# Optimization experiments

Hardware: AMD Instinct MI355X
Metric: run time of the kernel (lower is better)

The kernel has to match this reference:

```python
import jax, jax.numpy as jnp
import numpy as np

DIM = 1024
H_MID = max(8, DIM // 2)   # 512
H_LOW = max(8, DIM // 4)   # 256


def setup_inputs() -> dict:
    key = jax.random.key(0)
    ks = jax.random.split(key, 10)
    s = lambda fan_in: 1.0 / np.sqrt(fan_in)
    x = jax.random.normal(ks[0], (4, 8192, DIM), dtype=jnp.float32)
    return {
        "x": x,
        "gamma": jnp.ones((DIM,), jnp.float32),
        "beta": jnp.zeros((DIM,), jnp.float32),
        "W1": jax.random.uniform(ks[1], (DIM, H_MID), jnp.float32, -s(DIM), s(DIM)),
        "b1": jax.random.uniform(ks[2], (H_MID,), jnp.float32, -s(DIM), s(DIM)),
        "W2": jax.random.uniform(ks[3], (H_MID, H_MID), jnp.float32, -s(H_MID), s(H_MID)),
        "b2": jax.random.uniform(ks[4], (H_MID,), jnp.float32, -s(H_MID), s(H_MID)),
        "W3": jax.random.uniform(ks[5], (H_MID, H_LOW), jnp.float32, -s(H_MID), s(H_MID)),
        "b3": jax.random.uniform(ks[6], (H_LOW,), jnp.float32, -s(H_MID), s(H_MID)),
        "W4": jax.random.uniform(ks[7], (H_LOW, DIM), jnp.float32, -s(H_LOW), s(H_LOW)),
        "b4": jax.random.uniform(ks[8], (DIM,), jnp.float32, -s(H_LOW), s(H_LOW)),
    }


def _layernorm(x, gamma, beta, eps=1e-5):
    mu = jnp.mean(x, axis=-1, keepdims=True)
    var = jnp.mean(jnp.square(x - mu), axis=-1, keepdims=True)
    return (x - mu) * jax.lax.rsqrt(var + eps) * gamma + beta


def reference(x, gamma, beta, W1, b1, W2, b2, W3, b3, W4, b4):
    gelu = lambda h: jax.nn.gelu(h, approximate=False)  # torch default: exact erf GELU
    h = _layernorm(x, gamma, beta)                      # (B,S,D)
    h = gelu(jnp.einsum("bsd,dm->bsm", h, W1) + b1)    # (B,S,D/2)
    h = gelu(jnp.einsum("bsm,mn->bsn", h, W2) + b2)    # (B,S,D/2)
    h = gelu(jnp.einsum("bsn,nl->bsl", h, W3) + b3)    # (B,S,D/4)
    h = jnp.einsum("bsl,ld->bsd", h, W4) + b4          # (B,S,D)
    return x + h
```

## Files before the change

kernel.cpp:

```cpp
#include <hip/hip_runtime.h>


typedef short short8 __attribute__((ext_vector_type(8)));
typedef float floatx4 __attribute__((ext_vector_type(4)));
typedef unsigned short ushort4v __attribute__((ext_vector_type(4)));
typedef unsigned int uint2v __attribute__((ext_vector_type(2)));

__device__ __forceinline__ unsigned short f2bf(float f) {
    union { float f; unsigned int u; } a; a.f = f;
    unsigned int u = a.u;
    return (unsigned short)((u + 0x7FFFu + ((u >> 16) & 1u)) >> 16);
}

__device__ __forceinline__ float bf2f(unsigned short h) {
    union { unsigned int u; float f; } a; a.u = ((unsigned int)h) << 16;
    return a.f;
}

__device__ __forceinline__ unsigned int pkbf(float a, float b) {
    return (unsigned int)f2bf(a) | ((unsigned int)f2bf(b) << 16);
}

__device__ __forceinline__ float gelu_fast(float v) {
    float u = 0.7978845608f * v * (1.0f + 0.044715f * v * v);
    float e = __builtin_amdgcn_exp2f(u * 2.885390082f);
    float t = 1.0f - 2.0f * __builtin_amdgcn_rcpf(1.0f + e);
    return 0.5f * v * (1.0f + t);
}

__device__ __forceinline__ void gl_lds16(const unsigned short* g, unsigned short* l) {
    __builtin_amdgcn_global_load_lds(
        (const __attribute__((address_space(1))) void*)g,
        (__attribute__((address_space(3))) void*)l, 16, 0, 0);
}

#define BARX() asm volatile("s_barrier" ::: "memory")
#define VMW8() asm volatile("s_waitcnt vmcnt(8)" ::: "memory")
#define VMW4() asm volatile("s_waitcnt vmcnt(4)" ::: "memory")
#define VMW0() asm volatile("s_waitcnt vmcnt(0)" ::: "memory")

__global__ __launch_bounds__(256) void conv_all_kernel(
    const float* __restrict__ W1, const float* __restrict__ W2,
    const float* __restrict__ W3, const float* __restrict__ W4,
    const float* __restrict__ gamma, const float* __restrict__ b1,
    unsigned short* __restrict__ Wt1, unsigned short* __restrict__ Wt2,
    unsigned short* __restrict__ Wt3, unsigned short* __restrict__ Wt4,
    float* __restrict__ u1, float* __restrict__ c1) {
    int b = blockIdx.x;
    if (b >= 4608) {
        int n = (b - 4608) * 256 + threadIdx.x;
        u1[n] = 0.f;
        c1[n] = b1[n];
        return;
    }
    const float* W; unsigned short* Wt; int K, N; const float* sc = nullptr;
    if (b < 2048)      { W = W1; Wt = Wt1; K = 1024; N = 512;  sc = gamma; }
    else if (b < 3072) { W = W2; Wt = Wt2; K = 512;  N = 512;  b -= 2048; }
    else if (b < 3584) { W = W3; Wt = Wt3; K = 512;  N = 256;  b -= 3072; }
    else               { W = W4; Wt = Wt4; K = 256;  N = 1024; b -= 3584; }
    int t = b * 256 + threadIdx.x;
    int sh = 31 - __clz(N);
    int k = t >> sh, n = t & (N - 1);
    float v = W[t];
    if (sc) v *= sc[k];
    Wt[(size_t)n * K + k] = f2bf(v);
}

__global__ __launch_bounds__(256) void u1c1_kernel(
    const float* __restrict__ W1, const float* __restrict__ gamma,
    const float* __restrict__ beta, float* __restrict__ u1,
    float* __restrict__ c1) {
    const int N = 512;
    __shared__ float gs[16], bs[16];
    int n = threadIdx.x;
    int k0 = blockIdx.x * 16;
    if (n < 16) { gs[n] = gamma[k0 + n]; bs[n] = beta[k0 + n]; }
    __syncthreads();
    float ua = 0.f, ca = 0.f, ub = 0.f, cb = 0.f;
#pragma unroll
    for (int i = 0; i < 16; i++) {
        float w0 = W1[(size_t)(k0 + i) * N + n];
        float w1 = W1[(size_t)(k0 + i) * N + n + 256];
        ua += gs[i] * w0; ca += bs[i] * w0;
        ub += gs[i] * w1; cb += bs[i] * w1;
    }
    atomicAdd(&u1[n], ua);       atomicAdd(&c1[n], ca);
    atomicAdd(&u1[n + 256], ub); atomicAdd(&c1[n + 256], cb);
}

__global__ __launch_bounds__(256) void ln_stats_kernel(
    const float* __restrict__ x, float* __restrict__ mu, float* __restrict__ rs,
    unsigned short* __restrict__ xb) {
    const int D = 1024;
    int row = blockIdx.x * 4 + (threadIdx.x >> 6);
    int lane = threadIdx.x & 63;
    const float4* xr = (const float4*)(x + (size_t)row * D);
    float s = 0.f, ss = 0.f;
#pragma unroll
    for (int i = 0; i < 4; i++) {
        float4 v = xr[lane + 64 * i];
        s  += v.x + v.y + v.z + v.w;
        ss += v.x * v.x + v.y * v.y + v.z * v.z + v.w * v.w;
        if (xb) {
            ushort4v o;
            o.x = f2bf(v.x); o.y = f2bf(v.y); o.z = f2bf(v.z); o.w = f2bf(v.w);
            *(ushort4v*)(xb + (size_t)row * D + 4 * (lane + 64 * i)) = o;
        }
    }
#pragma unroll
    for (int off = 32; off; off >>= 1) {
        s  += __shfl_xor(s, off);
        ss += __shfl_xor(ss, off);
    }
    if (lane == 0) {
        float m = s * (1.0f / 1024.0f);
        mu[row] = m;
        rs[row] = rsqrtf(ss * (1.0f / 1024.0f) - m * m + 1e-5f);
    }
}

__device__ __forceinline__ void ldA8(const unsigned short* base, short8 (&a)[8]) {
#pragma unroll
    for (int mt = 0; mt < 8; mt++) a[mt] = *(const short8*)(base + mt * 512);
}
__device__ __forceinline__ void ldB2(const unsigned short* base, short8 (&bb)[2]) {
    bb[0] = *(const short8*)(base);
    bb[1] = *(const short8*)(base + 512);
}
template <int CH>
__device__ __forceinline__ void mm16(const short8 (&a)[8], const short8 (&bb)[2],
                                     floatx4 (&acc)[8][4]) {
    __builtin_amdgcn_s_setprio(1);
#pragma unroll
    for (int mt = 0; mt < 8; mt++)
#pragma unroll
        for (int nt = 0; nt < 2; nt++)
            acc[mt][CH * 2 + nt] = __builtin_amdgcn_mfma_f32_16x16x32_bf16(
                bb[nt], a[mt], acc[mt][CH * 2 + nt], 0, 0, 0);
    __builtin_amdgcn_s_setprio(0);
}

template <int KLEN, int MODE>
__device__ __forceinline__ void do_tile(
    const unsigned short* aF0, const unsigned short* bF0,
    const unsigned short* aF1, const unsigned short* bF1,
    unsigned short* sA3, unsigned short* sB3,
    unsigned short* sA4, unsigned short* sB4,
    const unsigned short* gAs, const unsigned short* gBs,
    short8 (&a)[8], short8 (&bb)[2], floatx4 (&acc)[8][4]) {
    ldA8(aF0, a);
    ldB2(bF0, bb);
    if (MODE <= 1) {
        gl_lds16(gAs + 96, sA3);
        gl_lds16(gAs + 96 + (size_t)128 * KLEN, sA3 + 4096);
    }
    mm16<0>(a, bb, acc);
    BARX();
    ldB2(bF0 + 1024, bb);
    if (MODE <= 1) {
        gl_lds16(gBs + 96, sB3);
        gl_lds16(gBs + 96 + (size_t)128 * KLEN, sB3 + 4096);
    }
    mm16<1>(a, bb, acc);
    if (MODE <= 1) { VMW8(); } else { VMW0(); }
    BARX();
    ldA8(aF1, a);
    ldB2(bF1, bb);
    if (MODE == 0) {
        gl_lds16(gAs + 128, sA4);
        gl_lds16(gAs + 128 + (size_t)128 * KLEN, sA4 + 4096);
    }
    mm16<0>(a, bb, acc);
    BARX();
    ldB2(bF1 + 1024, bb);
    if (MODE == 0) {
        gl_lds16(gBs + 128, sB4);
        gl_lds16(gBs + 128 + (size_t)128 * KLEN, sB4 + 4096);
    }
    mm16<1>(a, bb, acc);
    if (MODE == 0) { VMW8(); }
    else if (MODE == 1) { VMW4(); }
    BARX();
}

template <int EPMODE, int NBN, int NT, int NOUT, int KLEN>
__global__ __launch_bounds__(512, 2) void gemm256_kernel(
    const unsigned short* __restrict__ A, const unsigned short* __restrict__ Bt,
    unsigned short* __restrict__ Out,
    const float* __restrict__ bias,
    const float* __restrict__ u1,
    const float* __restrict__ mu,
    const float* __restrict__ rs)
{
    __shared__ unsigned short lds[4][2][8192];

    const int tid  = threadIdx.x;
    const int wave = tid >> 6;
    const int lane = tid & 63;
    const int q    = lane >> 4;
    const int l16  = lane & 15;
    const int wm   = wave >> 2;
    const int wn   = wave & 3;

    const int id   = blockIdx.x;
    const int xcd  = id & 7;
    const int slot = id >> 3;
    const int m0   = (xcd + 8 * (slot / NBN)) * 256;
    const int n0   = (slot % NBN) * 256;

    const unsigned short* gAs = A  + (size_t)(m0 + (tid >> 2)) * KLEN + (tid & 3) * 8;
    const unsigned short* gBs = Bt + (size_t)(n0 + (tid >> 2)) * KLEN + (tid & 3) * 8;

    const int wo = wave << 9;
    unsigned short* sA[4]; unsigned short* sB[4];
    const unsigned short* fA[4]; const unsigned short* fB[4];
    const int aoff = (wm * 128 + l16) * 32 + q * 8;
    const int boff = (wn * 64 + l16) * 32 + q * 8;
#pragma unroll
    for (int s = 0; s < 4; s++) {
        sA[s] = &lds[s][0][0] + wo;
        sB[s] = &lds[s][1][0] + wo;
        fA[s] = &lds[s][0][0] + aoff;
        fB[s] = &lds[s][1][0] + boff;
    }

    floatx4 acc[8][4] = {};
    short8 a[8], bb[2];

    gl_lds16(gAs,      sA[0]); gl_lds16(gAs      + (size_t)128 * KLEN, sA[0] + 4096);
    gl_lds16(gBs,      sB[0]); gl_lds16(gBs      + (size_t)128 * KLEN, sB[0] + 4096);
    gl_lds16(gAs + 32, sA[1]); gl_lds16(gAs + 32 + (size_t)128 * KLEN, sA[1] + 4096);
    gl_lds16(gBs + 32, sB[1]); gl_lds16(gBs + 32 + (size_t)128 * KLEN, sB[1] + 4096);
    gl_lds16(gAs + 64, sA[2]); gl_lds16(gAs + 64 + (size_t)128 * KLEN, sA[2] + 4096);
    gl_lds16(gBs + 64, sB[2]); gl_lds16(gBs + 64 + (size_t)128 * KLEN, sB[2] + 4096);
    VMW8();
    BARX();

    for (int t = 0; t + 2 < NT; t += 2) {
        do_tile<KLEN, 0>(fA[0], fB[0], fA[1], fB[1], sA[3], sB[3], sA[0], sB[0],
                         gAs, gBs, a, bb, acc);
        gAs += 64; gBs += 64;
        do_tile<KLEN, 0>(fA[2], fB[2], fA[3], fB[3], sA[1], sB[1], sA[2], sB[2],
                         gAs, gBs, a, bb, acc);
        gAs += 64; gBs += 64;
    }
    do_tile<KLEN, 1>(fA[0], fB[0], fA[1], fB[1], sA[3], sB[3], sA[0], sB[0],
                     gAs, gBs, a, bb, acc);
    gAs += 64; gBs += 64;
    do_tile<KLEN, 2>(fA[2], fB[2], fA[3], fB[3], sA[1], sB[1], sA[2], sB[2],
                     gAs, gBs, a, bb, acc);

    float rs8[8], mu8[8];
    if constexpr (EPMODE == 0) {
#pragma unroll
        for (int ma = 0; ma < 8; ma++) {
            const int row = m0 + wm * 128 + ma * 16 + l16;
            rs8[ma] = rs[row];
            mu8[ma] = mu[row];
        }
    }
#pragma unroll
    for (int na = 0; na < 4; na++) {
        const int nb = n0 + wn * 64 + na * 16 + q * 4;
        const float4 bv = *(const float4*)(bias + nb);
        float4 uv = {0.f, 0.f, 0.f, 0.f};
        if constexpr (EPMODE == 0) uv = *(const float4*)(u1 + nb);
#pragma unroll
        for (int ma = 0; ma < 8; ma++) {
            const int row = m0 + wm * 128 + ma * 16 + l16;
            const size_t off = (size_t)row * NOUT + nb;
            float v0 = acc[ma][na][0], v1 = acc[ma][na][1];
            float v2 = acc[ma][na][2], v3 = acc[ma][na][3];
            if constexpr (EPMODE == 0) {
                v0 = gelu_fast(rs8[ma] * (v0 - mu8[ma] * uv.x) + bv.x);
                v1 = gelu_fast(rs8[ma] * (v1 - mu8[ma] * uv.y) + bv.y);
                v2 = gelu_fast(rs8[ma] * (v2 - mu8[ma] * uv.z) + bv.z);
                v3 = gelu_fast(rs8[ma] * (v3 - mu8[ma] * uv.w) + bv.w);
            } else {
                v0 = gelu_fast(v0 + bv.x);
                v1 = gelu_fast(v1 + bv.y);
                v2 = gelu_fast(v2 + bv.z);
                v3 = gelu_fast(v3 + bv.w);
            }
            uint2v o; o.x = pkbf(v0, v1); o.y = pkbf(v2, v3);
            *(uint2v*)(Out + off) = o;
        }
    }
}

template <int EPMODE, bool AF32, int NBN, int NT_, int KT>
__global__ __launch_bounds__(256) void gemm_kernel(
    const void* __restrict__ Aptr, const unsigned short* __restrict__ Bt,
    void* __restrict__ Out,
    const float* __restrict__ bias,
    const float* __restrict__ u1,
    const float* __restrict__ mu,
    const float* __restrict__ rs,
    const void* __restrict__ resid)
{
    constexpr int BM = 128, BN = 128, BK = 64;
    constexpr int N = NT_, K = KT;
    __shared__ unsigned short As[BM][BK];
    __shared__ unsigned short Bs[BN][BK];

    const int tid  = threadIdx.x;
    const int wave = tid >> 6;
    const int lane = tid & 63;
    const int q    = lane >> 4;
    const int l16  = lane & 15;
    const int wm   = wave & 1;
    const int wn   = wave >> 1;

    const int id   = blockIdx.x;
    const int xcd  = id & 7;
    const int slot = id >> 3;
    const int m0   = (xcd + 8 * (slot / NBN)) * BM;
    const int n0   = (slot % NBN) * BN;

    const int sr  = tid >> 3;
    const int sc  = tid & 7;
    const int sg  = sc ^ (sr & 7);
    unsigned short* lA = &As[0][0] + (wave << 9);
    unsigned short* lB = &Bs[0][0] + (wave << 9);
    const unsigned short* gb0 = Bt + (size_t)(n0 + sr) * K + sg * 8;
    const unsigned short* ga0 = nullptr;
    if (!AF32) ga0 = (const unsigned short*)Aptr + (size_t)(m0 + sr) * K + sg * 8;

    floatx4 acc[4][4] = {};

#pragma unroll
    for (int k0 = 0; k0 < K; k0 += BK) {
        if (AF32) {
            const float* A = (const float*)Aptr;
            int c = tid & 15, r0 = tid >> 4;
#pragma unroll
            for (int i = 0; i < 8; i++) {
                int r = r0 + 16 * i;
                float4 v = *(const float4*)(A + (size_t)(m0 + r) * K + k0 + c * 4);
                ushort4v o;
                o.x = f2bf(v.x); o.y = f2bf(v.y);
                o.z = f2bf(v.z); o.w = f2bf(v.w);
                int idx = r * 64 + (((c >> 1) ^ (r & 7)) << 3) + ((c & 1) << 2);
                *(ushort4v*)(&As[0][0] + idx) = o;
            }
        } else {
#pragma unroll
            for (int c = 0; c < 4; c++)
                gl_lds16(ga0 + k0 + (size_t)(32 * c) * K, lA + c * 2048);
        }
#pragma unroll
        for (int c = 0; c < 4; c++)
            gl_lds16(gb0 + k0 + (size_t)(32 * c) * K, lB + c * 2048);
        __syncthreads();

#pragma unroll
        for (int kk = 0; kk < 2; kk++) {
            const int gsw = ((kk * 4 + q) ^ (l16 & 7)) * 8;
            short8 a[4], b[4];
#pragma unroll
            for (int mt = 0; mt < 4; mt++)
                a[mt] = *(const short8*)(&As[0][0] + (wm * 64 + mt * 16 + l16) * 64 + gsw);
#pragma unroll
            for (int nt = 0; nt < 4; nt++)
                b[nt] = *(const short8*)(&Bs[0][0] + (wn * 64 + nt * 16 + l16) * 64 + gsw);
#pragma unroll
            for (int nt = 0; nt < 4; nt++)
#pragma unroll
                for (int mt = 0; mt < 4; mt++)
                    acc[nt][mt] = __builtin_amdgcn_mfma_f32_16x16x32_bf16(
                        b[nt], a[mt], acc[nt][mt], 0, 0, 0);
        }
        __syncthreads();
    }

    float rs4[4], mu4[4];
    if constexpr (EPMODE == 0) {
#pragma unroll
        for (int mt = 0; mt < 4; mt++) {
            const int row = m0 + wm * 64 + mt * 16 + l16;
            rs4[mt] = rs[row];
            mu4[mt] = mu[row];
        }
    }
#pragma unroll
    for (int nt = 0; nt < 4; nt++) {
        const int nbase = n0 + wn * 64 + nt * 16 + q * 4;
        const float4 bv = *(const float4*)(bias + nbase);
        float4 uv = {0.f, 0.f, 0.f, 0.f};
        if constexpr (EPMODE == 0) uv = *(const float4*)(u1 + nbase);
#pragma unroll
        for (int mt = 0; mt < 4; mt++) {
            const int row = m0 + wm * 64 + mt * 16 + l16;
            const size_t off = (size_t)row * N + nbase;
            float v0 = acc[nt][mt][0], v1 = acc[nt][mt][1];
            float v2 = acc[nt][mt][2], v3 = acc[nt][mt][3];
            if constexpr (EPMODE == 0) {
                v0 = gelu_fast(rs4[mt] * (v0 - mu4[mt] * uv.x) + bv.x);
                v1 = gelu_fast(rs4[mt] * (v1 - mu4[mt] * uv.y) + bv.y);
                v2 = gelu_fast(rs4[mt] * (v2 - mu4[mt] * uv.z) + bv.z);
                v3 = gelu_fast(rs4[mt] * (v3 - mu4[mt] * uv.w) + bv.w);
                uint2v o; o.x = pkbf(v0, v1); o.y = pkbf(v2, v3);
                *(uint2v*)((unsigned short*)Out + off) = o;
            } else if constexpr (EPMODE == 1) {
                v0 = gelu_fast(v0 + bv.x);
                v1 = gelu_fast(v1 + bv.y);
                v2 = gelu_fast(v2 + bv.z);
                v3 = gelu_fast(v3 + bv.w);
                uint2v o; o.x = pkbf(v0, v1); o.y = pkbf(v2, v3);
                *(uint2v*)((unsigned short*)Out + off) = o;
            } else if constexpr (EPMODE == 2) {
                const float4 rv = *(const float4*)((const float*)resid + off);
                float4 o;
                o.x = v0 + bv.x + rv.x;
                o.y = v1 + bv.y + rv.y;
                o.z = v2 + bv.z + rv.z;
                o.w = v3 + bv.w + rv.w;
                *(float4*)((float*)Out + off) = o;
            } else {
                const ushort4v rv =
                    *(const ushort4v*)((const unsigned short*)resid + off);
                float4 o;
                o.x = v0 + bv.x + bf2f(rv.x);
                o.y = v1 + bv.y + bf2f(rv.y);
                o.z = v2 + bv.z + bf2f(rv.z);
                o.w = v3 + bv.w + bf2f(rv.w);
                *(float4*)((float*)Out + off) = o;
            }
        }
    }
}

extern "C" void kernel_launch(void* const* d_in, const int* in_sizes, int n_in,
                              void* d_out, int out_size, void* d_ws, size_t ws_size,
                              hipStream_t stream) {
    const float* x     = (const float*)d_in[0];
    const float* gamma = (const float*)d_in[1];
    const float* beta  = (const float*)d_in[2];
    const float* W1    = (const float*)d_in[3];
    const float* b1    = (const float*)d_in[4];
    const float* W2    = (const float*)d_in[5];
    const float* b2    = (const float*)d_in[6];
    const float* W3    = (const float*)d_in[7];
    const float* b3    = (const float*)d_in[8];
    const float* W4    = (const float*)d_in[9];
    const float* b4    = (const float*)d_in[10];
    float* out = (float*)d_out;

    const int D = 1024, H1 = 512, H2 = 512;
    const int M = in_sizes[0] / D;

    char* ws = (char*)d_ws;
    unsigned short* Wt1 = (unsigned short*)(ws + 0);
    unsigned short* Wt2 = (unsigned short*)(ws + 1048576);
    unsigned short* Wt3 = (unsigned short*)(ws + 1572864);
    unsigned short* Wt4 = (unsigned short*)(ws + 1835008);
    float* u1           = (float*)(ws + 2359296);
    float* c1           = (float*)(ws + 2361344);
    float* muv          = (float*)(ws + 2363392);
    float* rsv          = (float*)(ws + 2494464);
    unsigned short* h1  = (unsigned short*)(ws + 2625536);
    unsigned short* h2  = (unsigned short*)(ws + 36179968);
    unsigned short* h3  = h1;
    size_t base_end     = 36179968 + (size_t)M * H2 * 2;
    unsigned short* xb  = (unsigned short*)(ws + base_end);
    bool use_xb = (ws_size >= base_end + (size_t)M * D * 2);

    const int NBM = M / 128;

    conv_all_kernel<<<4610, 256, 0, stream>>>(W1, W2, W3, W4, gamma, b1,
                                              Wt1, Wt2, Wt3, Wt4, u1, c1);
    u1c1_kernel<<<D / 16, 256, 0, stream>>>(W1, gamma, beta, u1, c1);

    ln_stats_kernel<<<M / 4, 256, 0, stream>>>(x, muv, rsv, use_xb ? xb : nullptr);

    if (use_xb) {
        gemm256_kernel<0, 2, 16, 512, 1024><<<(M / 256) * 2, 512, 0, stream>>>(
            xb, Wt1, h1, c1, u1, muv, rsv);
    } else {
        gemm_kernel<0, true, 4, 512, 1024><<<4 * NBM, 256, 0, stream>>>(
            x, Wt1, h1, c1, u1, muv, rsv, nullptr);
    }
    gemm256_kernel<1, 2, 8, 512, 512><<<(M / 256) * 2, 512, 0, stream>>>(
        h1, Wt2, h2, b2, nullptr, nullptr, nullptr);
    gemm_kernel<1, false, 2, 256, 512><<<2 * NBM, 256, 0, stream>>>(
        h2, Wt3, h3, b3, nullptr, nullptr, nullptr, nullptr);
    if (use_xb) {
        gemm_kernel<3, false, 8, 1024, 256><<<8 * NBM, 256, 0, stream>>>(
            h3, Wt4, out, b4, nullptr, nullptr, nullptr, xb);
    } else {
        gemm_kernel<2, false, 8, 1024, 256><<<8 * NBM, 256, 0, stream>>>(
            h3, Wt4, out, b4, nullptr, nullptr, nullptr, x);
    }
}
```

Baseline: 399.0 us.

## Fuse GEMM2 and GEMM3 through LDS and merge LN stats into prep kernel

Adds a gemm23 kernel in which each 128-row block computes the full GELU(h1·W2+b2) tile into 128KB of LDS, then immediately multiplies it by W3 to produce h3. This removes the global round trip of the h2 intermediate and one launch. Separately, the layernorm-stats/bf16-cast work is folded into the weight-conversion kernel as extra blocks, which saves another launch. The fused GEMM is single-buffered with BK=32 and two barriers per step, and runs only one block per CU over M/128 blocks. That may make it less efficient than the previously tuned gemm256 path.

Result: no change. 404.0 us (+1.2%).

```diff
diff --git a/kernel.cpp b/kernel.cpp
--- a/kernel.cpp
+++ b/kernel.cpp
@@ -39,31 +39,63 @@
 #define VMW4() asm volatile("s_waitcnt vmcnt(4)" ::: "memory")
 #define VMW0() asm volatile("s_waitcnt vmcnt(0)" ::: "memory")
 
-__global__ __launch_bounds__(256) void conv_all_kernel(
+__global__ __launch_bounds__(256) void prep_kernel(
     const float* __restrict__ W1, const float* __restrict__ W2,
     const float* __restrict__ W3, const float* __restrict__ W4,
     const float* __restrict__ gamma, const float* __restrict__ b1,
+    const float* __restrict__ x,
     unsigned short* __restrict__ Wt1, unsigned short* __restrict__ Wt2,
     unsigned short* __restrict__ Wt3, unsigned short* __restrict__ Wt4,
-    float* __restrict__ u1, float* __restrict__ c1) {
+    float* __restrict__ u1, float* __restrict__ c1,
+    float* __restrict__ mu, float* __restrict__ rs,
+    unsigned short* __restrict__ xb) {
     int b = blockIdx.x;
-    if (b >= 4608) {
+    if (b < 4608) {
+        const float* W; unsigned short* Wt; int K, N; const float* sc = nullptr;
+        if (b < 2048)      { W = W1; Wt = Wt1; K = 1024; N = 512;  sc = gamma; }
+        else if (b < 3072) { W = W2; Wt = Wt2; K = 512;  N = 512;  b -= 2048; }
+        else if (b < 3584) { W = W3; Wt = Wt3; K = 512;  N = 256;  b -= 3072; }
+        else               { W = W4; Wt = Wt4; K = 256;  N = 1024; b -= 3584; }
+        int t = b * 256 + threadIdx.x;
+        int sh = 31 - __clz(N);
+        int k = t >> sh, n = t & (N - 1);
+        float v = W[t];
+        if (sc) v *= sc[k];
+        Wt[(size_t)n * K + k] = f2bf(v);
+        return;
+    }
+    if (b < 4610) {
         int n = (b - 4608) * 256 + threadIdx.x;
         u1[n] = 0.f;
         c1[n] = b1[n];
         return;
     }
-    const float* W; unsigned short* Wt; int K, N; const float* sc = nullptr;
-    if (b < 2048)      { W = W1; Wt = Wt1; K = 1024; N = 512;  sc = gamma; }
-    else if (b < 3072) { W = W2; Wt = Wt2; K = 512;  N = 512;  b -= 2048; }
-    else if (b < 3584) { W = W3; Wt = Wt3; K = 512;  N = 256;  b -= 3072; }
-    else               { W = W4; Wt = Wt4; K = 256;  N = 1024; b -= 3584; }
-    int t = b * 256 + threadIdx.x;
-    int sh = 31 - __clz(N);
-    int k = t >> sh, n = t & (N - 1);
-    float v = W[t];
-    if (sc) v *= sc[k];
-    Wt[(size_t)n * K + k] = f2bf(v);
+    const int D = 1024;
+    int row = (b - 4610) * 4 + (threadIdx.x >> 6);
+    int lane = threadIdx.x & 63;
+    const float4* xr = (const float4*)(x + (size_t)row * D);
+    float s = 0.f, ss = 0.f;
+#pragma unroll
+    for (int i = 0; i < 4; i++) {
+        float4 v = xr[lane + 64 * i];
+        s  += v.x + v.y + v.z + v.w;
+        ss += v.x * v.x + v.y * v.y + v.z * v.z + v.w * v.w;
+        if (xb) {
+            ushort4v o;
+            o.x = f2bf(v.x); o.y = f2bf(v.y); o.z = f2bf(v.z); o.w = f2bf(v.w);
+            *(ushort4v*)(xb + (size_t)row * D + 4 * (lane + 64 * i)) = o;
+        }
+    }
+#pragma unroll
+    for (int off = 32; off; off >>= 1) {
+        s  += __shfl_xor(s, off);
+        ss += __shfl_xor(ss, off);
+    }
+    if (lane == 0) {
+        float m = s * (1.0f / 1024.0f);
+        mu[row] = m;
+        rs[row] = rsqrtf(ss * (1.0f / 1024.0f) - m * m + 1e-5f);
+    }
 }
 
 __global__ __launch_bounds__(256) void u1c1_kernel(
@@ -86,37 +118,6 @@
     }
     atomicAdd(&u1[n], ua);       atomicAdd(&c1[n], ca);
     atomicAdd(&u1[n + 256], ub); atomicAdd(&c1[n + 256], cb);
-}
-
-__global__ __launch_bounds__(256) void ln_stats_kernel(
-    const float* __restrict__ x, float* __restrict__ mu, float* __restrict__ rs,
-    unsigned short* __restrict__ xb) {
-    const int D = 1024;
-    int row = blockIdx.x * 4 + (threadIdx.x >> 6);
-    int lane = threadIdx.x & 63;
-    const float4* xr = (const float4*)(x + (size_t)row * D);
-    float s = 0.f, ss = 0.f;
-#pragma unroll
-    for (int i = 0; i < 4; i++) {
-        float4 v = xr[lane + 64 * i];
-        s  += v.x + v.y + v.z + v.w;
-        ss += v.x * v.x + v.y * v.y + v.z * v.z + v.w * v.w;
-        if (xb) {
-            ushort4v o;
-            o.x = f2bf(v.x); o.y = f2bf(v.y); o.z = f2bf(v.z); o.w = f2bf(v.w);
-            *(ushort4v*)(xb + (size_t)row * D + 4 * (lane + 64 * i)) = o;
-        }
-    }
-#pragma unroll
-    for (int off = 32; off; off >>= 1) {
-        s  += __shfl_xor(s, off);
-        ss += __shfl_xor(ss, off);
-    }
-    if (lane == 0) {
-        float m = s * (1.0f / 1024.0f);
-        mu[row] = m;
-        rs[row] = rsqrtf(ss * (1.0f / 1024.0f) - m * m + 1e-5f);
-    }
 }
 
 __device__ __forceinline__ void ldA8(const unsigned short* base, short8 (&a)[8]) {
@@ -284,6 +285,112 @@
             }
             uint2v o; o.x = pkbf(v0, v1); o.y = pkbf(v2, v3);
             *(uint2v*)(Out + off) = o;
+        }
+    }
+}
+
+__global__ __launch_bounds__(512, 2) void gemm23_kernel(
+    const unsigned short* __restrict__ h1, const unsigned short* __restrict__ Wt2,
+    const unsigned short* __restrict__ Wt3, unsigned short* __restrict__ h3,
+    const float* __restrict__ b2, const float* __restrict__ b3)
+{
+    __shared__ unsigned short h2s[65536];
+    __shared__ unsigned short stg[8192];
+    const int tid  = threadIdx.x;
+    const int wave = tid >> 6, lane = tid & 63;
+    const int q = lane >> 4, l16 = lane & 15;
+    const int wm = wave >> 2, wn = wave & 3;
+    const int m0 = blockIdx.x * 128;
+    const int sr2 = tid >> 2, pg2 = tid & 3;
+    const int sg2 = pg2 ^ (sr2 & 3);
+    unsigned short* stW0 = stg + wave * 512;
+    unsigned short* stW1 = stg + 4096 + wave * 512;
+    const int x2 = (q ^ (l16 & 3)) * 8;
+
+    floatx4 acc[4][4];
+    short8 a[4], bb[4];
+
+    for (int nt4 = 0; nt4 < 4; nt4++) {
+#pragma unroll
+        for (int mt = 0; mt < 4; mt++)
+#pragma unroll
+            for (int nt = 0; nt < 2; nt++)
+                acc[mt][nt] = (floatx4){0.f, 0.f, 0.f, 0.f};
+        for (int ks = 0; ks < 16; ks++) {
+            gl_lds16(h1  + (size_t)(m0 + sr2) * 512        + ks * 32 + sg2 * 8, stW0);
+            gl_lds16(Wt2 + (size_t)(nt4 * 128 + sr2) * 512 + ks * 32 + sg2 * 8, stW1);
+            __syncthreads();
+#pragma unroll
+            for (int mt = 0; mt < 4; mt++)
+                a[mt] = *(const short8*)(stg + (wm * 64 + mt * 16 + l16) * 32 + x2);
+#pragma unroll
+            for (int nt = 0; nt < 2; nt++)
+                bb[nt] = *(const short8*)(stg + 4096 + (wn * 32 + nt * 16 + l16) * 32 + x2);
+#pragma unroll
+            for (int mt = 0; mt < 4; mt++)
+#pragma unroll
+                for (int nt = 0; nt < 2; nt++)
+                    acc[mt][nt] = __builtin_amdgcn_mfma_f32_16x16x32_bf16(
+                        bb[nt], a[mt], acc[mt][nt], 0, 0, 0);
+            __syncthreads();
+        }
+#pragma unroll
+        for (int nt = 0; nt < 2; nt++) {
+            const int col = nt4 * 128 + wn * 32 + nt * 16 + q * 4;
+            const float4 bv = *(const float4*)(b2 + col);
+#pragma unroll
+            for (int mt = 0; mt < 4; mt++) {
+                const int row = wm * 64 + mt * 16 + l16;
+                float v0 = gelu_fast(acc[mt][nt][0] + bv.x);
+                float v1 = gelu_fast(acc[mt][nt][1] + bv.y);
+                float v2 = gelu_fast(acc[mt][nt][2] + bv.z);
+                float v3 = gelu_fast(acc[mt][nt][3] + bv.w);
+                const int phys = (col >> 3) ^ (l16 & 7);
+                uint2v o; o.x = pkbf(v0, v1); o.y = pkbf(v2, v3);
+                *(uint2v*)(h2s + row * 512 + phys * 8 + (q & 1) * 4) = o;
+            }
+        }
+    }
+
+#pragma unroll
+    for (int mt = 0; mt < 4; mt++)
+#pragma unroll
+        for (int nt = 0; nt < 4; nt++)
+            acc[mt][nt] = (floatx4){0.f, 0.f, 0.f, 0.f};
+    for (int ks = 0; ks < 16; ks++) {
+        gl_lds16(Wt3 + (size_t)(sr2) * 512       + ks * 32 + sg2 * 8, stW0);
+        gl_lds16(Wt3 + (size_t)(sr2 + 128) * 512 + ks * 32 + sg2 * 8, stW1);
+        __syncthreads();
+#pragma unroll
+        for (int mt = 0; mt < 4; mt++) {
+            const int row = wm * 64 + mt * 16 + l16;
+            const int phys = (ks * 4 + q) ^ (l16 & 7);
+            a[mt] = *(const short8*)(h2s + row * 512 + phys * 8);
+        }
+#pragma unroll
+        for (int nt = 0; nt < 4; nt++)
+            bb[nt] = *(const short8*)(stg + (wn * 64 + nt * 16 + l16) * 32 + x2);
+#pragma unroll
+        for (int mt = 0; mt < 4; mt++)
+#pragma unroll
+            for (int nt = 0; nt < 4; nt++)
+                acc[mt][nt] = __builtin_amdgcn_mfma_f32_16x16x32_bf16(
+                    bb[nt], a[mt], acc[mt][nt], 0, 0, 0);
+        __syncthreads();
+    }
+#pragma unroll
+    for (int nt = 0; nt < 4; nt++) {
+        const int col = wn * 64 + nt * 16 + q * 4;
+        const float4 bv = *(const float4*)(b3 + col);
+#pragma unroll
+        for (int mt = 0; mt < 4; mt++) {
+            const int row = m0 + wm * 64 + mt * 16 + l16;
+            float v0 = gelu_fast(acc[mt][nt][0] + bv.x);
+            float v1 = gelu_fast(acc[mt][nt][1] + bv.y);
+            float v2 = gelu_fast(acc[mt][nt][2] + bv.z);
+            float v3 = gelu_fast(acc[mt][nt][3] + bv.w);
+            uint2v o; o.x = pkbf(v0, v1); o.y = pkbf(v2, v3);
+            *(uint2v*)(h3 + (size_t)row * 256 + col) = o;
         }
     }
 }
@@ -459,20 +566,17 @@
     float* muv          = (float*)(ws + 2363392);
     float* rsv          = (float*)(ws + 2494464);
     unsigned short* h1  = (unsigned short*)(ws + 2625536);
-    unsigned short* h2  = (unsigned short*)(ws + 36179968);
-    unsigned short* h3  = h1;
+    unsigned short* h3  = (unsigned short*)(ws + 36179968);
     size_t base_end     = 36179968 + (size_t)M * H2 * 2;
     unsigned short* xb  = (unsigned short*)(ws + base_end);
     bool use_xb = (ws_size >= base_end + (size_t)M * D * 2);
 
     const int NBM = M / 128;
 
-    conv_all_kernel<<<4610, 256, 0, stream>>>(W1, W2, W3, W4, gamma, b1,
-                                              Wt1, Wt2, Wt3, Wt4, u1, c1);
+    prep_kernel<<<4610 + M / 4, 256, 0, stream>>>(
+        W1, W2, W3, W4, gamma, b1, x, Wt1, Wt2, Wt3, Wt4,
+        u1, c1, muv, rsv, use_xb ? xb : nullptr);
     u1c1_kernel<<<D / 16, 256, 0, stream>>>(W1, gamma, beta, u1, c1);
-
-    ln_stats_kernel<<<M / 4, 256, 0, stream>>>(x, muv, rsv, use_xb ? xb : nullptr);
-
     if (use_xb) {
         gemm256_kernel<0, 2, 16, 512, 1024><<<(M / 256) * 2, 512, 0, stream>>>(
             xb, Wt1, h1, c1, u1, muv, rsv);
@@ -480,10 +584,7 @@
         gemm_kernel<0, true, 4, 512, 1024><<<4 * NBM, 256, 0, stream>>>(
             x, Wt1, h1, c1, u1, muv, rsv, nullptr);
     }
-    gemm256_kernel<1, 2, 8, 512, 512><<<(M / 256) * 2, 512, 0, stream>>>(
-        h1, Wt2, h2, b2, nullptr, nullptr, nullptr);
-    gemm_kernel<1, false, 2, 256, 512><<<2 * NBM, 256, 0, stream>>>(
-        h2, Wt3, h3, b3, nullptr, nullptr, nullptr, nullptr);
+    gemm23_kernel<<<M / 128, 512, 0, stream>>>(h1, Wt2, Wt3, h3, b2, b3);
     if (use_xb) {
         gemm_kernel<3, false, 8, 1024, 256><<<8 * NBM, 256, 0, stream>>>(
             h3, Wt4, out, b4, nullptr, nullptr, nullptr, xb);
```
